# Performance work log

Hardware: AMD Instinct MI355X
Metric: run time of the kernel (lower is better)

## Reference

```python
import jax, jax.numpy as jnp
import numpy as np

M_NUMS = 4096
D_NUMS = 4096
PROJ = 256
EPS = 1e-10


def _lin(x, W, b):
    # torch nn.Linear: y = x @ W.T + b
    return x @ W.T + b


def setup_inputs() -> dict:
    key = jax.random.key(0)
    ks = jax.random.split(key, 16)
    N = M_NUMS + D_NUMS
    inp = {}
    inp["m_d_feat"] = jax.random.normal(ks[0], (N, PROJ), dtype=jnp.float32)
    inp["bigraph"] = jax.random.uniform(ks[1], (N, N), dtype=jnp.float32)
    # sparse-ish binary co-occurrence matrices (values !=0 / ==0 drive masks)
    inp["m_co"] = (jax.random.uniform(ks[2], (M_NUMS, M_NUMS)) < 0.1).astype(jnp.float32)
    inp["d_co"] = (jax.random.uniform(ks[3], (D_NUMS, D_NUMS)) < 0.1).astype(jnp.float32)
    # positive degrees in [1, 50) to keep 1/sqrt and 1/deg well-conditioned
    inp["m_co_deg"] = jax.random.uniform(ks[4], (M_NUMS, 2)) * 49.0 + 1.0
    inp["d_co_deg"] = jax.random.uniform(ks[5], (D_NUMS, 2)) * 49.0 + 1.0
    inp["m_d_degree"] = jax.random.uniform(ks[6], (M_NUMS,)) * 49.0 + 1.0
    inp["d_m_degree"] = jax.random.uniform(ks[7], (D_NUMS,)) * 49.0 + 1.0
    s = 0.02
    inp["Wm"] = jax.random.normal(ks[8], (3, PROJ, PROJ), dtype=jnp.float32) * s
    inp["bm"] = jnp.zeros((3, PROJ), dtype=jnp.float32)
    inp["Wd"] = jax.random.normal(ks[9], (3, PROJ, PROJ), dtype=jnp.float32) * s
    inp["bd"] = jnp.zeros((3, PROJ), dtype=jnp.float32)
    inp["Wx"] = jax.random.normal(ks[10], (8, PROJ, PROJ), dtype=jnp.float32) * s
    inp["bx"] = jnp.zeros((8, PROJ), dtype=jnp.float32)
    inp["central_m"] = jax.random.randint(ks[11], (M_NUMS,), 0, 2, dtype=jnp.int32)
    inp["central_d"] = jax.random.randint(ks[12], (D_NUMS,), 0, 2, dtype=jnp.int32)
    inp["m_nums"] = M_NUMS
    return inp


def _homog_block(feat, co, deg, W, b):
    # self-loop + degree-normalized co-occurrence / non-co-occurrence GEMMs
    n = feat.shape[0]
    diag = jnp.eye(n, dtype=bool)
    co_mask = (~diag) & (co != 0)
    non_mask = (~diag) & (co == 0)
    out = _lin(feat, W[0], b[0])  # self loop
    d0 = deg[:, 0]
    coeff0 = (1.0 / jnp.sqrt(d0[:, None] * d0[None, :] + EPS)) * co_mask.astype(feat.dtype)
    out = out + coeff0 @ _lin(feat, W[1], b[1])
    d1 = deg[:, 1]
    coeff1 = (1.0 / jnp.sqrt(d1[:, None] * d1[None, :] + EPS)) * non_mask.astype(feat.dtype)
    out = out + coeff1 @ _lin(feat, W[2], b[2])
    return out


def _cross_block(assoc, row_central, col_central, norm_row, src_feat, Wx, bx, pairs):
    # sum of 4 (central/normal x central/normal) masked-association GEMMs
    rc = row_central != 0
    cc = col_central != 0
    masks = [
        rc[:, None] & cc[None, :],
        rc[:, None] & (~cc)[None, :],
        (~rc)[:, None] & cc[None, :],
        (~rc)[:, None] & (~cc)[None, :],
    ]
    norm = (1.0 / norm_row)[:, None]
    out = jnp.zeros((assoc.shape[0], src_feat.shape[1]), dtype=src_feat.dtype)
    for mask, (i, j) in zip(masks, pairs):
        transformed = _lin(src_feat, Wx[i], bx[i]) + _lin(src_feat, Wx[j], bx[j])
        out = out + 0.5 * norm * ((assoc * mask.astype(assoc.dtype)) @ transformed)
    return out


def reference(m_d_feat, bigraph, m_co, m_co_deg, d_co, d_co_deg, m_d_degree,
              d_m_degree, Wm, bm, Wd, bd, Wx, bx, central_m, central_d, m_nums):
    m = m_nums
    m_feat = m_d_feat[:m]
    d_feat = m_d_feat[m:]

    out_m = _homog_block(m_feat, m_co, m_co_deg, Wm, bm)
    out_d = _homog_block(d_feat, d_co, d_co_deg, Wd, bd)

    # m <- d aggregation: Wx indices 0..7 =
    # [cm2cd, cd2cm, cm2nd, cd2nm, nm2cd, nd2cm, nm2nd, nd2nm]
    assoc_md = bigraph[:m, m:]
    out_m = out_m + _cross_block(assoc_md, central_m, central_d, m_d_degree,
                                 d_feat, Wx, bx,
                                 pairs=[(0, 1), (2, 5), (4, 3), (6, 7)])
    # d <- m aggregation (roles swapped)
    assoc_dm = bigraph[m:, :m]
    out_d = out_d + _cross_block(assoc_dm, central_d, central_m, d_m_degree,
                                 m_feat, Wx, bx,
                                 pairs=[(1, 0), (3, 4), (5, 2), (7, 6)])

    return jnp.concatenate([out_m, out_d], axis=0)
```

## Files before the change

kernel.cpp:

```cpp
#include <hip/hip_runtime.h>
#include <hip/hip_bf16.h>


typedef __bf16 bf16x8 __attribute__((ext_vector_type(8)));
typedef float floatx4 __attribute__((ext_vector_type(4)));
using bf16 = __hip_bfloat16;

#define LDK 72

__device__ __forceinline__ float b2f(bf16 x){ return __bfloat162float(x); }
__device__ __forceinline__ bf16 f2b(float f){ return __float2bfloat16(f); }
__device__ __forceinline__ float rawb2f(unsigned short u){
  unsigned int x = ((unsigned int)u) << 16; float f; __builtin_memcpy(&f,&x,4); return f;
}
__device__ __forceinline__ unsigned short f2bu(float f){
  bf16 h = __float2bfloat16(f); unsigned short u; __builtin_memcpy(&u,&h,2); return u;
}
__device__ __forceinline__ uint4 cvt8(float4 a, float4 b){
  unsigned short u[8] = {f2bu(a.x),f2bu(a.y),f2bu(a.z),f2bu(a.w),
                         f2bu(b.x),f2bu(b.y),f2bu(b.z),f2bu(b.w)};
  uint4 v; __builtin_memcpy(&v,u,16); return v;
}
__device__ __forceinline__ void async_ld16(const void* gp, void* lp){
  typedef __attribute__((address_space(1))) const unsigned int GU;
  typedef __attribute__((address_space(3))) unsigned int LU;
  __builtin_amdgcn_global_load_lds((GU*)(unsigned long long)gp,
                                   (LU*)(unsigned int)(unsigned long long)lp,
                                   16, 0, 0);
}

__global__ void prep_kernel(const float* __restrict__ m_co_deg, const float* __restrict__ d_co_deg,
                            const float* __restrict__ m_d_degree, const float* __restrict__ d_m_degree,
                            const float* __restrict__ Wx, const float* __restrict__ bx,
                            float* __restrict__ scal, float* __restrict__ Sbuf, float* __restrict__ bSbuf)
{
  const int i = blockIdx.x*blockDim.x + threadIdx.x;
  if (i < 4096){
    scal[0*4096+i] = rsqrtf(m_co_deg[2*i]);
    scal[1*4096+i] = rsqrtf(m_co_deg[2*i+1]);
    scal[2*4096+i] = 0.5f / m_d_degree[i];
    scal[3*4096+i] = rsqrtf(d_co_deg[2*i]);
    scal[4*4096+i] = rsqrtf(d_co_deg[2*i+1]);
    scal[5*4096+i] = 0.5f / d_m_degree[i];
  }
  const int pa[4] = {0,2,3,6}, pb[4] = {1,5,4,7};
  if (i < 65536){
    #pragma unroll
    for (int s=0;s<4;s++)
      Sbuf[s*65536+i] = Wx[pa[s]*65536+i] + Wx[pb[s]*65536+i];
  }
  if (i < 256){
    #pragma unroll
    for (int s=0;s<4;s++)
      bSbuf[s*256+i] = bx[pa[s]*256+i] + bx[pb[s]*256+i];
  }
}

__global__ __launch_bounds__(256) void stage1_kernel(
    const float* __restrict__ feat, const float* __restrict__ Wm, const float* __restrict__ bm,
    const float* __restrict__ Wd, const float* __restrict__ bd,
    const float* __restrict__ Sbuf, const float* __restrict__ bSbuf, const float* __restrict__ scal,
    bf16* __restrict__ BHm, bf16* __restrict__ BHd,
    float* __restrict__ L0m, float* __restrict__ L0d,
    float* __restrict__ L2nm, float* __restrict__ L2nd,
    bf16* __restrict__ Tm, bf16* __restrict__ Td)
{
  __shared__ __align__(16) bf16 As[128*LDK];
  __shared__ __align__(16) bf16 Bs[128*LDK];
  const int p = blockIdx.y;
  const int side = p >> 3, widx = p & 7;
  const int bx_ = blockIdx.x;
  const bool modeT = (widx != 0 && widx != 7);
  const float* X = feat + (size_t)side*(4096*256);
  const float* Wb = side ? Wd : Wm;
  const float* W = (widx==0) ? Wb : (widx==7) ? (Wb + 2*65536)
                 : (widx<=2) ? (Wb + widx*65536) : (Sbuf + (widx-3)*65536);
  int rt, ct;
  if (!modeT){ rt = bx_>>1; ct = bx_&1; } else { rt = bx_&1; ct = bx_>>1; }
  const float* Amat = modeT ? W : X;
  const float* Bmat = modeT ? X : W;
  const int arow0 = rt*128, brow0 = ct*128;
  const int tid = threadIdx.x;
  const int lane = tid & 63, wv = tid>>6;
  const int wr = wv>>1, wc = wv&1, q = lane>>4, l15 = lane&15;

  floatx4 acc[4][4];
  #pragma unroll
  for (int i=0;i<4;i++)
    #pragma unroll
    for (int j=0;j<4;j++)
      #pragma unroll
      for (int r=0;r<4;r++) acc[i][j][r] = 0.f;

  for (int kt=0; kt<4; kt++){
    const int c0 = kt*64;
    __syncthreads();
    #pragma unroll
    for (int i=0;i<4;i++){
      const int id = tid + i*256;
      const int row = id>>3, kg = id&7;
      const float* ap = Amat + (size_t)(arow0+row)*256 + c0 + kg*8;
      const float* bp = Bmat + (size_t)(brow0+row)*256 + c0 + kg*8;
      float4 a0 = *(const float4*)ap, a1 = *(const float4*)(ap+4);
      float4 b0 = *(const float4*)bp, b1 = *(const float4*)(bp+4);
      *(uint4*)(&As[row*LDK + kg*8]) = cvt8(a0,a1);
      *(uint4*)(&Bs[row*LDK + kg*8]) = cvt8(b0,b1);
    }
    __syncthreads();
    #pragma unroll
    for (int ki=0; ki<2; ki++){
      bf16x8 af[4], bg[4];
      #pragma unroll
      for (int i=0;i<4;i++) af[i] = *(const bf16x8*)&As[(wr*64 + i*16 + l15)*LDK + ki*32 + q*8];
      #pragma unroll
      for (int j=0;j<4;j++) bg[j] = *(const bf16x8*)&Bs[(wc*64 + j*16 + l15)*LDK + ki*32 + q*8];
      #pragma unroll
      for (int i=0;i<4;i++)
        #pragma unroll
        for (int j=0;j<4;j++)
          acc[i][j] = __builtin_amdgcn_mfma_f32_16x16x32_bf16(af[i], bg[j], acc[i][j], 0,0,0);
    }
  }

  const float* bb = side ? bd : bm;
  const float* bias = (widx==0) ? bb : (widx==7) ? (bb + 512)
                    : (widx<=2) ? (bb + widx*256) : (bSbuf + (widx-3)*256);
  float* outF = nullptr; bf16* outB = nullptr; int pitch = 256; const float* scl = nullptr;
  if (widx==0){ outF = side? L0d : L0m; }
  else if (widx==7){ outF = side? L2nd : L2nm; }
  else if (widx==1){ outB = side? BHd : BHm; pitch = 4096; scl = scal + side*12288; }
  else if (widx==2){ outB = (side? BHd : BHm) + 256*4096; pitch = 4096; scl = scal + side*12288 + 4096; }
  else { outB = (side? Td : Tm) + (widx-3)*(256*4096); pitch = 4096; }

  #pragma unroll
  for (int i=0;i<4;i++){
    #pragma unroll
    for (int j=0;j<4;j++){
      const int gcol = brow0 + wc*64 + j*16 + l15;
      #pragma unroll
      for (int r=0;r<4;r++){
        const int grow = arow0 + wr*64 + i*16 + q*4 + r;
        float v = acc[i][j][r];
        const int nidx = modeT ? grow : gcol;
        v += bias[nidx];
        if (scl) v *= scl[gcol];
        if (outF) outF[(size_t)grow*pitch + gcol] = v;
        else      outB[(size_t)grow*pitch + gcol] = f2b(v);
      }
    }
  }
}

__global__ void stage2_kernel(const bf16* __restrict__ Tm, const bf16* __restrict__ Td,
                              const int* __restrict__ central_m, const int* __restrict__ central_d,
                              bf16* __restrict__ BXm, bf16* __restrict__ BXd)
{
  const int idx = blockIdx.x*blockDim.x + threadIdx.x;
  const int oside = idx >> 20;
  const int rem = idx & 1048575;
  const int n = rem >> 12;
  const int c = rem & 4095;
  const bf16* T = oside ? Tm : Td;
  const int* cen = oside ? central_m : central_d;
  bf16* B = oside ? BXd : BXm;
  const bool cc = cen[c] != 0;
  int v0i, v1i;
  if (!oside){ v0i = cc ? 2 : 3; v1i = cc ? 0 : 1; }
  else       { v0i = cc ? 1 : 3; v1i = cc ? 0 : 2; }
  const float v0 = b2f(T[(size_t)v0i*1048576 + (size_t)n*4096 + c]);
  const float v1 = b2f(T[(size_t)v1i*1048576 + (size_t)n*4096 + c]);
  B[(size_t)n*4096 + c]         = f2b(v0);
  B[(size_t)(256+n)*4096 + c]   = f2b(v1 - v0);
}

__global__ void colsum_kernel(const bf16* __restrict__ BHm, const bf16* __restrict__ BHd,
                              float* __restrict__ Scol)
{
  const int b = blockIdx.x;
  const int sd = b >> 8, n = b & 255;
  const int lane = threadIdx.x;
  const bf16* rowp = (sd ? BHd : BHm) + (size_t)(256+n)*4096;
  float s = 0.f;
  #pragma unroll
  for (int t=0;t<8;t++){
    const uint4 v = *(const uint4*)(rowp + t*512 + lane*8);
    unsigned short u[8]; __builtin_memcpy(u,&v,16);
    #pragma unroll
    for (int jj=0;jj<8;jj++) s += rawb2f(u[jj]);
  }
  #pragma unroll
  for (int off=32; off>0; off>>=1) s += __shfl_down(s, off);
  if (lane==0) Scol[sd*256 + n] = s;
}

__global__ void zero_kernel(float* __restrict__ p)
{
  const size_t idx = (size_t)blockIdx.x*blockDim.x + threadIdx.x;
  float4 z = {0.f,0.f,0.f,0.f};
  #pragma unroll
  for (int t=0;t<4;t++) *(float4*)(p + (idx + (size_t)t*262144)*4) = z;
}

__global__ __launch_bounds__(256,2) void gemm_kernel(
    const float* __restrict__ bigraph, const float* __restrict__ m_co, const float* __restrict__ d_co,
    const int* __restrict__ central_m, const int* __restrict__ central_d,
    const float* __restrict__ scal,
    const bf16* __restrict__ BHm, const bf16* __restrict__ BHd,
    const bf16* __restrict__ BXm, const bf16* __restrict__ BXd,
    float* __restrict__ partial)
{
  __shared__ __align__(16) bf16 As[8192];
  __shared__ __align__(16) bf16 Bs[2][8192];
  const int bid = blockIdx.x;
  const int seg = bid & 1, nt = (bid>>1)&1, mt = (bid>>2)&31, p = bid>>7;
  const int s = p & 1;
  const bool maskmode = (p < 2);
  const int k0 = seg*2048;
  const int rowbase = mt*128;
  const int n0 = nt*128;
  const float* Asrc; int apitch; int acoff;
  if (p==0){ Asrc = m_co; apitch = 4096; acoff = 0; }
  else if (p==1){ Asrc = d_co; apitch = 4096; acoff = 0; }
  else if (p==2){ Asrc = bigraph; apitch = 8192; acoff = 4096; }
  else { Asrc = bigraph + (size_t)4096*8192; apitch = 8192; acoff = 0; }
  const bf16* B0 = (p==0) ? BHm : (p==1) ? BHd : (p==2) ? BXm : BXd;

  const int tid = threadIdx.x;
  const int lane = tid&63, wv = tid>>6, wr = wv>>1, wc = wv&1, q = lane>>4, l15 = lane&15;

  floatx4 acc0[4][4], acc1[4][4];
  #pragma unroll
  for (int i=0;i<4;i++)
    #pragma unroll
    for (int j=0;j<4;j++)
      #pragma unroll
      for (int r=0;r<4;r++){ acc0[i][j][r] = 0.f; acc1[i][j][r] = 0.f; }

  for (int kt=0; kt<32; kt++){
    const int kkg = k0 + kt*64;
    #pragma unroll
    for (int g2=0; g2<2; g2++){
      #pragma unroll
      for (int j=0;j<4;j++){
        const int chunk = wv*256 + j*64 + lane;
        const int row = chunk >> 3, sg = chunk & 7;
        const int gg = sg ^ (row & 7);
        const bf16* gp = B0 + (size_t)(g2*256 + n0 + row)*4096 + kkg + gg*8;
        async_ld16(gp, &Bs[g2][(wv*256 + j*64)*8]);
      }
    }
    #pragma unroll
    for (int i=0;i<4;i++){
      const int chunk = i*256 + tid;
      const int row = chunk >> 3, sg = chunk & 7;
      const int g = sg ^ (row & 7);
      const int gr = rowbase + row;
      const float* ap = Asrc + (size_t)gr*apitch + acoff + kkg + g*8;
      float4 a0 = *(const float4*)ap, a1 = *(const float4*)(ap+4);
      const float av[8] = {a0.x,a0.y,a0.z,a0.w,a1.x,a1.y,a1.z,a1.w};
      unsigned short u[8];
      if (maskmode){
        const int cbase = kkg + g*8;
        #pragma unroll
        for (int jj=0;jj<8;jj++)
          u[jj] = (av[jj]!=0.0f && (cbase+jj)!=gr) ? (unsigned short)0x3F80 : (unsigned short)0;
      } else {
        #pragma unroll
        for (int jj=0;jj<8;jj++) u[jj] = f2bu(av[jj]);
      }
      uint4 w4; __builtin_memcpy(&w4,u,16);
      *(uint4*)(&As[chunk*8]) = w4;
    }
    __syncthreads();
    #pragma unroll
    for (int ki=0; ki<2; ki++){
      bf16x8 af[4], b0f[4], b1f[4];
      #pragma unroll
      for (int i=0;i<4;i++){
        const int ra = wr*64 + i*16 + l15;
        af[i] = *(const bf16x8*)&As[ra*64 + ((ki*4+q)^(ra&7))*8];
      }
      #pragma unroll
      for (int j=0;j<4;j++){
        const int rb = wc*64 + j*16 + l15;
        const int off = rb*64 + ((ki*4+q)^(rb&7))*8;
        b0f[j] = *(const bf16x8*)&Bs[0][off];
        b1f[j] = *(const bf16x8*)&Bs[1][off];
      }
      #pragma unroll
      for (int i=0;i<4;i++)
        #pragma unroll
        for (int j=0;j<4;j++){
          acc0[i][j] = __builtin_amdgcn_mfma_f32_16x16x32_bf16(af[i], b0f[j], acc0[i][j], 0,0,0);
          acc1[i][j] = __builtin_amdgcn_mfma_f32_16x16x32_bf16(af[i], b1f[j], acc1[i][j], 0,0,0);
        }
    }
    __syncthreads();
  }

  const float* scS = scal + (size_t)s*12288;
  const int* cenR = s ? central_d : central_m;
  float* pb = partial + (size_t)p*4096*256;
  #pragma unroll
  for (int i=0;i<4;i++){
    #pragma unroll
    for (int r_=0;r_<4;r_++){
      const int rl = rowbase + wr*64 + i*16 + q*4 + r_;
      float w0, w1;
      if (maskmode){ w0 = scS[rl]; w1 = -scS[4096+rl]; }
      else { const float nr = scS[8192+rl]; w0 = nr; w1 = cenR[rl] ? nr : 0.f; }
      #pragma unroll
      for (int j=0;j<4;j++){
        const int gcol = n0 + wc*64 + j*16 + l15;
        atomicAdd(&pb[(size_t)rl*256 + gcol], w0*acc0[i][j][r_] + w1*acc1[i][j][r_]);
      }
    }
  }
}

__global__ void reduce_kernel(const float* __restrict__ partial,
                              const float* __restrict__ L0m, const float* __restrict__ L0d,
                              const float* __restrict__ L2nm, const float* __restrict__ L2nd,
                              const float* __restrict__ Scol, const float* __restrict__ scal,
                              float* __restrict__ out)
{
  const int idx = blockIdx.x*blockDim.x + threadIdx.x;
  const int r = idx >> 6;
  const int n4 = (idx & 63) << 2;
  const int s = r >> 12;
  const int rl = r & 4095;
  const float r1 = scal[s*12288 + 4096 + rl];
  const size_t rb = (size_t)rl*256 + n4;
  const float4 l0 = *(const float4*)((s? L0d : L0m) + rb);
  const float4 l2 = *(const float4*)((s? L2nd : L2nm) + rb);
  const float4 sc = *(const float4*)(Scol + s*256 + n4);
  const float4 ph = *(const float4*)(partial + (size_t)s*1048576 + rb);
  const float4 px = *(const float4*)(partial + (size_t)(2+s)*1048576 + rb);
  const float r1sq = r1*r1;
  float4 o;
  o.x = l0.x + ph.x + px.x + r1*sc.x - r1sq*l2.x;
  o.y = l0.y + ph.y + px.y + r1*sc.y - r1sq*l2.y;
  o.z = l0.z + ph.z + px.z + r1*sc.z - r1sq*l2.z;
  o.w = l0.w + ph.w + px.w + r1*sc.w - r1sq*l2.w;
  *(float4*)(out + (size_t)r*256 + n4) = o;
}

extern "C" void kernel_launch(void* const* d_in, const int* in_sizes, int n_in,
                              void* d_out, int out_size, void* d_ws, size_t ws_size,
                              hipStream_t stream)
{
  (void)in_sizes; (void)n_in; (void)out_size; (void)ws_size;
  const float* m_d_feat   = (const float*)d_in[0];
  const float* bigraph    = (const float*)d_in[1];
  const float* m_co       = (const float*)d_in[2];
  const float* d_co       = (const float*)d_in[3];
  const float* m_co_deg   = (const float*)d_in[4];
  const float* d_co_deg   = (const float*)d_in[5];
  const float* m_d_degree = (const float*)d_in[6];
  const float* d_m_degree = (const float*)d_in[7];
  const float* Wm = (const float*)d_in[8];
  const float* bm = (const float*)d_in[9];
  const float* Wd = (const float*)d_in[10];
  const float* bd = (const float*)d_in[11];
  const float* Wx = (const float*)d_in[12];
  const float* bx = (const float*)d_in[13];
  const int* central_m = (const int*)d_in[14];
  const int* central_d = (const int*)d_in[15];

  char* ws = (char*)d_ws;
  bf16*  BHm  = (bf16*) (ws + 0);
  bf16*  BHd  = (bf16*) (ws + 4194304);
  bf16*  BXm  = (bf16*) (ws + 8388608);
  bf16*  BXd  = (bf16*) (ws + 12582912);
  float* L0m  = (float*)(ws + 16777216);
  float* L0d  = (float*)(ws + 20971520);
  float* L2nm = (float*)(ws + 25165824);
  float* L2nd = (float*)(ws + 29360128);
  float* Sbuf = (float*)(ws + 33554432);
  float* bSbuf= (float*)(ws + 34603008);
  float* scal = (float*)(ws + 34607104);
  float* Scol = (float*)(ws + 34705408);
  bf16*  Tm   = (bf16*) (ws + 34707456);
  bf16*  Td   = (bf16*) (ws + 43096064);
  float* partial = (float*)(ws + 34707456);

  prep_kernel<<<256, 256, 0, stream>>>(m_co_deg, d_co_deg, m_d_degree, d_m_degree,
                                       Wx, bx, scal, Sbuf, bSbuf);
  stage1_kernel<<<dim3(64,16), 256, 0, stream>>>(m_d_feat, Wm, bm, Wd, bd, Sbuf, bSbuf, scal,
                                                 BHm, BHd, L0m, L0d, L2nm, L2nd, Tm, Td);
  stage2_kernel<<<8192, 256, 0, stream>>>(Tm, Td, central_m, central_d, BXm, BXd);
  colsum_kernel<<<512, 64, 0, stream>>>(BHm, BHd, Scol);
  zero_kernel<<<1024, 256, 0, stream>>>(partial);
  gemm_kernel<<<512, 256, 0, stream>>>(bigraph, m_co, d_co, central_m, central_d,
                                       scal, BHm, BHd, BXm, BXd, partial);
  reduce_kernel<<<2048, 256, 0, stream>>>(partial, L0m, L0d, L2nm, L2nd, Scol, scal, (float*)d_out);
}
```

Baseline: 601.1 us.

## Restructure GEMM to 512-thread blocks covering full N with double-buffered K=32 tiles

The main GEMM kernel now uses 512 threads (8 waves, 2x4 arrangement) and each block covers all 256 output columns. Previously the N dimension was split across two blocks, so the fp32 A matrix was read and converted twice; now it is read once. The K split goes from 2 to 4 segments, and the K tile shrinks from 64 to 32 with LDS double buffering, so the next tile's loads overlap the current tile's MFMAs. A block-index swizzle spreads work across XCDs. The cost is more atomic partial adds, from more K segments, plus higher register and LDS pressure per block.

```diff
diff --git a/kernel.cpp b/kernel.cpp
--- a/kernel.cpp
+++ b/kernel.cpp
@@ -201,7 +201,7 @@
   for (int t=0;t<4;t++) *(float4*)(p + (idx + (size_t)t*262144)*4) = z;
 }
 
-__global__ __launch_bounds__(256,2) void gemm_kernel(
+__global__ __launch_bounds__(512,2) void gemm_kernel(
     const float* __restrict__ bigraph, const float* __restrict__ m_co, const float* __restrict__ d_co,
     const int* __restrict__ central_m, const int* __restrict__ central_d,
     const float* __restrict__ scal,
@@ -209,15 +209,15 @@
     const bf16* __restrict__ BXm, const bf16* __restrict__ BXd,
     float* __restrict__ partial)
 {
-  __shared__ __align__(16) bf16 As[8192];
-  __shared__ __align__(16) bf16 Bs[2][8192];
+  __shared__ __align__(16) bf16 As[2][128*32];
+  __shared__ __align__(16) bf16 Bs[2][512*32];
   const int bid = blockIdx.x;
-  const int seg = bid & 1, nt = (bid>>1)&1, mt = (bid>>2)&31, p = bid>>7;
+  const int w = (bid & 7)*64 + (bid >> 3);
+  const int seg = w & 3, mt = (w >> 2) & 31, p = w >> 7;
   const int s = p & 1;
   const bool maskmode = (p < 2);
-  const int k0 = seg*2048;
+  const int k0 = seg*1024;
   const int rowbase = mt*128;
-  const int n0 = nt*128;
   const float* Asrc; int apitch; int acoff;
   if (p==0){ Asrc = m_co; apitch = 4096; acoff = 0; }
   else if (p==1){ Asrc = d_co; apitch = 4096; acoff = 0; }
@@ -226,7 +226,9 @@
   const bf16* B0 = (p==0) ? BHm : (p==1) ? BHd : (p==2) ? BXm : BXd;
 
   const int tid = threadIdx.x;
-  const int lane = tid&63, wv = tid>>6, wr = wv>>1, wc = wv&1, q = lane>>4, l15 = lane&15;
+  const int lane = tid&63, wv = tid>>6;
+  const int wr = wv>>2, wc = wv&3;
+  const int q = lane>>4, l15 = lane&15;
 
   floatx4 acc0[4][4], acc1[4][4];
   #pragma unroll
@@ -236,24 +238,21 @@
       #pragma unroll
       for (int r=0;r<4;r++){ acc0[i][j][r] = 0.f; acc1[i][j][r] = 0.f; }
 
-  for (int kt=0; kt<32; kt++){
-    const int kkg = k0 + kt*64;
-    #pragma unroll
-    for (int g2=0; g2<2; g2++){
-      #pragma unroll
-      for (int j=0;j<4;j++){
-        const int chunk = wv*256 + j*64 + lane;
-        const int row = chunk >> 3, sg = chunk & 7;
-        const int gg = sg ^ (row & 7);
-        const bf16* gp = B0 + (size_t)(g2*256 + n0 + row)*4096 + kkg + gg*8;
-        async_ld16(gp, &Bs[g2][(wv*256 + j*64)*8]);
-      }
-    }
-    #pragma unroll
-    for (int i=0;i<4;i++){
-      const int chunk = i*256 + tid;
-      const int row = chunk >> 3, sg = chunk & 7;
-      const int g = sg ^ (row & 7);
+  auto stage = [&](int kt, int buf){
+    const int kkg = k0 + kt*32;
+    #pragma unroll
+    for (int j=0;j<4;j++){
+      const int cb = wv*256 + j*64;
+      const int chunk = cb + lane;
+      const int row = chunk>>2, sg = chunk&3;
+      const int gg = sg ^ ((row>>1)&3);
+      const bf16* gp = B0 + (size_t)row*4096 + kkg + gg*8;
+      async_ld16(gp, &Bs[buf][cb*8]);
+    }
+    {
+      const int chunk = tid;
+      const int row = chunk>>2, sg = chunk&3;
+      const int g = sg ^ ((row>>1)&3);
       const int gr = rowbase + row;
       const float* ap = Asrc + (size_t)gr*apitch + acoff + kkg + g*8;
       float4 a0 = *(const float4*)ap, a1 = *(const float4*)(ap+4);
@@ -269,31 +268,33 @@
         for (int jj=0;jj<8;jj++) u[jj] = f2bu(av[jj]);
       }
       uint4 w4; __builtin_memcpy(&w4,u,16);
-      *(uint4*)(&As[chunk*8]) = w4;
-    }
-    __syncthreads();
-    #pragma unroll
-    for (int ki=0; ki<2; ki++){
-      bf16x8 af[4], b0f[4], b1f[4];
+      *(uint4*)(&As[buf][chunk*8]) = w4;
+    }
+  };
+
+  stage(0, 0);
+  __syncthreads();
+
+  for (int kt=0; kt<32; kt++){
+    const int cur = kt & 1;
+    if (kt+1 < 32) stage(kt+1, cur^1);
+    bf16x8 af[4];
+    #pragma unroll
+    for (int i=0;i<4;i++){
+      const int ra = wr*64 + i*16 + l15;
+      af[i] = *(const bf16x8*)&As[cur][ra*32 + ((q ^ ((ra>>1)&3)))*8];
+    }
+    #pragma unroll
+    for (int j=0;j<4;j++){
+      const int rb = wc*64 + j*16 + l15;
+      const int off = rb*32 + ((q ^ ((rb>>1)&3)))*8;
+      const bf16x8 b0 = *(const bf16x8*)&Bs[cur][off];
+      const bf16x8 b1 = *(const bf16x8*)&Bs[cur][256*32 + off];
       #pragma unroll
       for (int i=0;i<4;i++){
-        const int ra = wr*64 + i*16 + l15;
-        af[i] = *(const bf16x8*)&As[ra*64 + ((ki*4+q)^(ra&7))*8];
+        acc0[i][j] = __builtin_amdgcn_mfma_f32_16x16x32_bf16(af[i], b0, acc0[i][j], 0,0,0);
+        acc1[i][j] = __builtin_amdgcn_mfma_f32_16x16x32_bf16(af[i], b1, acc1[i][j], 0,0,0);
       }
-      #pragma unroll
-      for (int j=0;j<4;j++){
-        const int rb = wc*64 + j*16 + l15;
-        const int off = rb*64 + ((ki*4+q)^(rb&7))*8;
-        b0f[j] = *(const bf16x8*)&Bs[0][off];
-        b1f[j] = *(const bf16x8*)&Bs[1][off];
-      }
-      #pragma unroll
-      for (int i=0;i<4;i++)
-        #pragma unroll
-        for (int j=0;j<4;j++){
-          acc0[i][j] = __builtin_amdgcn_mfma_f32_16x16x32_bf16(af[i], b0f[j], acc0[i][j], 0,0,0);
-          acc1[i][j] = __builtin_amdgcn_mfma_f32_16x16x32_bf16(af[i], b1f[j], acc1[i][j], 0,0,0);
-        }
     }
     __syncthreads();
   }
@@ -311,7 +312,7 @@
       else { const float nr = scS[8192+rl]; w0 = nr; w1 = cenR[rl] ? nr : 0.f; }
       #pragma unroll
       for (int j=0;j<4;j++){
-        const int gcol = n0 + wc*64 + j*16 + l15;
+        const int gcol = wc*64 + j*16 + l15;
         atomicAdd(&pb[(size_t)rl*256 + gcol], w0*acc0[i][j][r_] + w1*acc1[i][j][r_]);
       }
     }
@@ -391,7 +392,7 @@
   stage2_kernel<<<8192, 256, 0, stream>>>(Tm, Td, central_m, central_d, BXm, BXd);
   colsum_kernel<<<512, 64, 0, stream>>>(BHm, BHd, Scol);
   zero_kernel<<<1024, 256, 0, stream>>>(partial);
-  gemm_kernel<<<512, 256, 0, stream>>>(bigraph, m_co, d_co, central_m, central_d,
+  gemm_kernel<<<512, 512, 0, stream>>>(bigraph, m_co, d_co, central_m, central_d,
                                        scal, BHm, BHd, BXm, BXd, partial);
   reduce_kernel<<<2048, 256, 0, stream>>>(partial, L0m, L0d, L2nm, L2nd, Scol, scal, (float*)d_out);
 }
```

Result: no change. 611.9 us (+1.8%).
